# Optimization experiments

Measured on AMD Instinct MI355X. Metric: run time of the kernel, lower is better.

Reference implementation:

```python
import jax, jax.numpy as jnp
import numpy as np

IN_CH, OUT_CH, K, STRIDE = 128, 256, 3, 1

def setup_inputs() -> dict:
    key = jax.random.key(0)
    kx, kw = jax.random.split(key)
    x = jax.random.normal(kx, (32, IN_CH, 56, 56), dtype=jnp.float32)
    # xavier_uniform: bound = sqrt(6 / (fan_in + fan_out)), fans include receptive field
    fan_in = IN_CH * K * K
    fan_out = OUT_CH * K * K
    bound = float(np.sqrt(6.0 / (fan_in + fan_out)))
    weight = jax.random.uniform(kw, (OUT_CH, IN_CH, K, K), dtype=jnp.float32,
                                minval=-bound, maxval=bound)
    bias = jnp.zeros((OUT_CH,), dtype=jnp.float32)
    return {"x": x, "weight": weight, "bias": bias}

def reference(x, weight, bias):
    # VALID (no-padding) conv, stride STRIDE, NCHW layout, OIHW kernel
    out = jax.lax.conv_general_dilated(
        x, weight,
        window_strides=(STRIDE, STRIDE),
        padding="VALID",
        dimension_numbers=("NCHW", "OIHW", "NCHW"))
    return out + bias[None, :, None, None]
```

## Files before the change

### kernel.cpp

```cpp
#include <hip/hip_runtime.h>
#include <hip/hip_bf16.h>
#include <stdint.h>

#define NB    32
#define CIN   128
#define HIN   56
#define HW    (HIN*HIN)
#define OCH   256
#define OHW   54
#define SPB   (OHW*OHW)
#define KSZ   (CIN*9)
#define BM    256
#define BN    128
#define BK    32
#define NKS   (KSZ/BK)
#define TOTC  (NB*SPB)
#define NT    729
#define GRAN  1536

typedef __attribute__((ext_vector_type(8))) short bf16x8;
typedef __attribute__((ext_vector_type(4))) float f32x4;

typedef __attribute__((address_space(1))) const uint32_t g_u32;
typedef __attribute__((address_space(3))) uint32_t l_u32;
static __device__ __forceinline__ void gl_lds16(const void* g, void* l) {
    __builtin_amdgcn_global_load_lds((g_u32*)g, (l_u32*)l, 16, 0, 0);
}

__global__ void xpose_cast(const float* __restrict__ x, __hip_bfloat16* __restrict__ xt) {
    __shared__ float tile[32][33];
    const int hw0 = blockIdx.x * 32;
    const int c0  = blockIdx.y * 32;
    const int n   = blockIdx.z;
    const int tx = threadIdx.x, ty = threadIdx.y;
    const float* xp = x + ((size_t)n*CIN + c0)*HW + hw0;
    #pragma unroll
    for (int i = ty; i < 32; i += 8)
        tile[i][tx] = xp[(size_t)i*HW + tx];
    __syncthreads();
    const int t = ty*32 + tx;
    const int hwl = t >> 3, q = t & 7;
    ushort4 v;
    v.x = __bfloat16_as_ushort(__float2bfloat16(tile[q*4+0][hwl]));
    v.y = __bfloat16_as_ushort(__float2bfloat16(tile[q*4+1][hwl]));
    v.z = __bfloat16_as_ushort(__float2bfloat16(tile[q*4+2][hwl]));
    v.w = __bfloat16_as_ushort(__float2bfloat16(tile[q*4+3][hwl]));
    __hip_bfloat16* op = xt + ((size_t)n*HW + hw0 + hwl)*CIN + c0 + q*4;
    *(ushort4*)op = v;
}

__global__ void wcast(const float* __restrict__ w, __hip_bfloat16* __restrict__ wt) {
    int tid = blockIdx.x*256 + threadIdx.x;
    if (tid >= OCH*KSZ) return;
    int oc = tid / KSZ, r = tid % KSZ;
    int pos = r >> 7, ic = r & 127;
    wt[tid] = __float2bfloat16(w[((size_t)(oc*CIN + ic))*9 + pos]);
}

__global__ __launch_bounds__(256, 2)
void conv_mfma(const __hip_bfloat16* __restrict__ xt,
               const __hip_bfloat16* __restrict__ wt,
               const float* __restrict__ bias,
               float* __restrict__ out) {
    __shared__ uint4 smem[3*GRAN];

    const int t = threadIdx.x;
    const int orig = blockIdx.x;
    const int xcd = orig & 7;
    const int tile = (xcd < 1 ? xcd*92 : 92 + (xcd-1)*91) + (orig >> 3);

    const int lane = t & 63, wid = t >> 6;
    const int wm = wid >> 1, wn = wid & 1;
    const int lr = lane & 15, lq = lane >> 4;

    const __hip_bfloat16* asrc[4];
    #pragma unroll
    for (int i = 0; i < 4; ++i) {
        int q = i*256 + t;
        int row = q >> 2, j = q & 3;
        int ls = j ^ ((row >> 1) & 3);
        asrc[i] = wt + (size_t)row*KSZ + ls*8;
    }
    const __hip_bfloat16* bsrc[2];
    #pragma unroll
    for (int i = 0; i < 2; ++i) {
        int q = i*256 + t;
        int col = q >> 2, j = q & 3;
        int ls = j ^ ((col >> 1) & 3);
        int colg = tile*BN + col;
        int n = colg / SPB, rem = colg - n*SPB;
        int oh = rem / OHW, ow = rem - oh*OHW;
        bsrc[i] = xt + ((size_t)(n*HIN + oh)*HIN + ow)*CIN + ls*8;
    }

    auto issueT = [&](uint4* dst, int ks) {
        const int aoff = ks*BK;
        const int pos = ks >> 2;
        const int kh = pos / 3, kw = pos - kh*3;
        const int boff = (kh*HIN + kw)*CIN + (ks & 3)*32;
        #pragma unroll
        for (int i = 0; i < 4; ++i) gl_lds16(asrc[i] + aoff, dst + i*256 + t);
        #pragma unroll
        for (int i = 0; i < 2; ++i) gl_lds16(bsrc[i] + boff, dst + 1024 + i*256 + t);
    };

    int ao[8], bo[4];
    #pragma unroll
    for (int mi = 0; mi < 8; ++mi) {
        int ra = wm*128 + mi*16 + lr;
        ao[mi] = ra*4 + (lq ^ ((ra >> 1) & 3));
    }
    #pragma unroll
    for (int ni = 0; ni < 4; ++ni) {
        int cb = wn*64 + ni*16 + lr;
        bo[ni] = 1024 + cb*4 + (lq ^ ((cb >> 1) & 3));
    }

    f32x4 acc[8][4];
    #pragma unroll
    for (int i = 0; i < 8; ++i)
        #pragma unroll
        for (int j = 0; j < 4; ++j)
            acc[i][j] = (f32x4){0.f, 0.f, 0.f, 0.f};

    #define MFMA_BF16 __builtin_amdgcn_mfma_f32_16x16x32_bf16
    #define RD_AABB(AA, BB, P) \
        _Pragma("unroll") for (int mi = 0; mi < 4; ++mi) AA[mi] = *(bf16x8*)&(P)[ao[mi]]; \
        _Pragma("unroll") for (int ni = 0; ni < 4; ++ni) BB[ni] = *(bf16x8*)&(P)[bo[ni]];
    #define RD_AB(AB, P) \
        _Pragma("unroll") for (int mi = 0; mi < 4; ++mi) AB[mi] = *(bf16x8*)&(P)[ao[4 + mi]];
    #define MFMA16LO(AA, BB) \
        _Pragma("unroll") for (int mi = 0; mi < 4; ++mi) \
            _Pragma("unroll") for (int ni = 0; ni < 4; ++ni) \
                acc[mi][ni] = MFMA_BF16(AA[mi], BB[ni], acc[mi][ni], 0, 0, 0);
    #define MFMA16HI(AB, BB) \
        _Pragma("unroll") for (int mi = 0; mi < 4; ++mi) \
            _Pragma("unroll") for (int ni = 0; ni < 4; ++ni) \
                acc[4+mi][ni] = MFMA_BF16(AB[mi], BB[ni], acc[4+mi][ni], 0, 0, 0);
    #define SCHEDB __builtin_amdgcn_sched_barrier(0)

    uint4 *bcur = smem, *bnext = smem + GRAN, *bthird = smem + 2*GRAN;
    bf16x8 aaE[4], abE[4], bbE[4];
    bf16x8 aaO[4], abO[4], bbO[4];

    issueT(bcur, 0); issueT(bnext, 1);
    asm volatile("s_waitcnt vmcnt(6)" ::: "memory");
    __builtin_amdgcn_s_barrier();
    SCHEDB;
    RD_AABB(aaE, bbE, bcur)
    RD_AB(abE, bcur)

    for (int ks = 0; ks < NKS; ks += 2) {
        asm volatile("s_waitcnt vmcnt(0)" ::: "memory");
        __builtin_amdgcn_s_barrier();
        SCHEDB;
        if (ks + 2 < NKS) issueT(bthird, ks + 2);
        RD_AABB(aaO, bbO, bnext)
        asm volatile("s_waitcnt lgkmcnt(8)" ::: "memory");
        SCHEDB;
        MFMA16LO(aaE, bbE)
        RD_AB(abO, bnext)
        MFMA16HI(abE, bbE)
        { uint4* tmp = bcur; bcur = bnext; bnext = bthird; bthird = tmp; }

        asm volatile("s_waitcnt vmcnt(0)" ::: "memory");
        __builtin_amdgcn_s_barrier();
        SCHEDB;
        if (ks + 3 < NKS) issueT(bthird, ks + 3);
        if (ks + 2 < NKS) {
            RD_AABB(aaE, bbE, bnext)
            asm volatile("s_waitcnt lgkmcnt(8)" ::: "memory");
        } else {
            asm volatile("s_waitcnt lgkmcnt(0)" ::: "memory");
        }
        SCHEDB;
        MFMA16LO(aaO, bbO)
        if (ks + 2 < NKS) { RD_AB(abE, bnext) }
        MFMA16HI(abO, bbO)
        { uint4* tmp = bcur; bcur = bnext; bnext = bthird; bthird = tmp; }
    }

    __syncthreads();

    float (*eps)[132] = (float (*)[132])smem;
    const int cl4 = (t & 31) * 4;
    const int rsub = t >> 5;
    const int colg = tile*BN + cl4;
    const int nn = colg / SPB;
    const int sp = colg - nn*SPB;
    #pragma unroll
    for (int h = 0; h < 4; ++h) {
        if (wm == (h >> 1)) {
            const int mib = (h & 1) * 4;
            #pragma unroll
            for (int ii = 0; ii < 4; ++ii) {
                int rl = ii*16 + lq*4;
                #pragma unroll
                for (int ni = 0; ni < 4; ++ni) {
                    int cl = wn*64 + ni*16 + lr;
                    #pragma unroll
                    for (int r = 0; r < 4; ++r)
                        eps[rl + r][cl] = acc[mib + ii][ni][r];
                }
            }
        }
        __syncthreads();
        {
            #pragma unroll
            for (int pass = 0; pass < 8; ++pass) {
                int rl = pass*8 + rsub;
                int rg = h*64 + rl;
                f32x4 v = *(f32x4*)&eps[rl][cl4];
                v = v + bias[rg];
                *(f32x4*)&out[((size_t)nn*OCH + rg)*SPB + sp] = v;
            }
        }
        __syncthreads();
    }
}

__global__ void conv_naive(const float* __restrict__ x, const float* __restrict__ w,
                           const float* __restrict__ bias, float* __restrict__ out) {
    size_t tid = (size_t)blockIdx.x*256 + threadIdx.x;
    const size_t total = (size_t)NB*OCH*SPB;
    if (tid >= total) return;
    int col = (int)(tid % SPB);
    int oc  = (int)((tid / SPB) % OCH);
    int n   = (int)(tid / ((size_t)SPB*OCH));
    int oh = col / OHW, ow = col % OHW;
    float s = bias[oc];
    for (int ic = 0; ic < CIN; ++ic)
        #pragma unroll
        for (int kh = 0; kh < 3; ++kh)
            #pragma unroll
            for (int kw = 0; kw < 3; ++kw)
                s += x[((size_t)(n*CIN+ic)*HIN + oh+kh)*HIN + ow+kw]
                   * w[((size_t)(oc*CIN+ic)*3 + kh)*3 + kw];
    out[tid] = s;
}

extern "C" void kernel_launch(void* const* d_in, const int* in_sizes, int n_in,
                              void* d_out, int out_size, void* d_ws, size_t ws_size,
                              hipStream_t stream) {
    const float* x    = (const float*)d_in[0];
    const float* w    = (const float*)d_in[1];
    const float* bias = (const float*)d_in[2];
    float* out = (float*)d_out;

    const size_t xt_bytes = (size_t)NB*HW*CIN*sizeof(__hip_bfloat16);
    const size_t wt_bytes = (size_t)OCH*KSZ*sizeof(__hip_bfloat16);

    if (ws_size >= xt_bytes + wt_bytes) {
        __hip_bfloat16* xt  = (__hip_bfloat16*)d_ws;
        __hip_bfloat16* wtp = (__hip_bfloat16*)((char*)d_ws + xt_bytes);
        hipLaunchKernelGGL(xpose_cast, dim3(HW/32, CIN/32, NB), dim3(32, 8), 0, stream, x, xt);
        hipLaunchKernelGGL(wcast, dim3((OCH*KSZ + 255)/256), dim3(256), 0, stream, w, wtp);
        hipLaunchKernelGGL(conv_mfma, dim3(NT), dim3(256), 0, stream, xt, wtp, bias, out);
    } else {
        size_t total = (size_t)NB*OCH*SPB;
        hipLaunchKernelGGL(conv_naive, dim3((unsigned)((total + 255)/256)), dim3(256), 0, stream,
                           x, w, bias, out);
    }
}
```

Baseline: 96.31 us.

## Reorder pipelined main loop to overlap LDS reads with MFMA and raise MFMA priority

Restructures the triple-buffered K loop. Each half-step now issues the global prefetch, runs the first MFMA group, reads the next stage's full fragment set from LDS, runs the second MFMA group, and ends with a combined vmcnt/lgkmcnt drain plus barrier. Barriers previously came before the LDS reads; now they come after compute, so LDS reads overlap with MFMAs. It also wraps the MFMA blocks in s_setprio(1)/s_setprio(0) to favour matrix issue across waves, at the cost of full drains at each barrier and more live fragment registers.

```diff
diff --git a/kernel.cpp b/kernel.cpp
--- a/kernel.cpp
+++ b/kernel.cpp
@@ -124,60 +124,52 @@
             acc[i][j] = (f32x4){0.f, 0.f, 0.f, 0.f};
 
     #define MFMA_BF16 __builtin_amdgcn_mfma_f32_16x16x32_bf16
-    #define RD_AABB(AA, BB, P) \
+    #define RDSET(AA, AB, BB, P) \
         _Pragma("unroll") for (int mi = 0; mi < 4; ++mi) AA[mi] = *(bf16x8*)&(P)[ao[mi]]; \
-        _Pragma("unroll") for (int ni = 0; ni < 4; ++ni) BB[ni] = *(bf16x8*)&(P)[bo[ni]];
-    #define RD_AB(AB, P) \
+        _Pragma("unroll") for (int ni = 0; ni < 4; ++ni) BB[ni] = *(bf16x8*)&(P)[bo[ni]]; \
         _Pragma("unroll") for (int mi = 0; mi < 4; ++mi) AB[mi] = *(bf16x8*)&(P)[ao[4 + mi]];
-    #define MFMA16LO(AA, BB) \
+    #define MFMA16(AARR, BARR, MIB) \
+        __builtin_amdgcn_s_setprio(1); \
         _Pragma("unroll") for (int mi = 0; mi < 4; ++mi) \
             _Pragma("unroll") for (int ni = 0; ni < 4; ++ni) \
-                acc[mi][ni] = MFMA_BF16(AA[mi], BB[ni], acc[mi][ni], 0, 0, 0);
-    #define MFMA16HI(AB, BB) \
-        _Pragma("unroll") for (int mi = 0; mi < 4; ++mi) \
-            _Pragma("unroll") for (int ni = 0; ni < 4; ++ni) \
-                acc[4+mi][ni] = MFMA_BF16(AB[mi], BB[ni], acc[4+mi][ni], 0, 0, 0);
+                acc[(MIB)+mi][ni] = MFMA_BF16(AARR[mi], BARR[ni], acc[(MIB)+mi][ni], 0, 0, 0); \
+        __builtin_amdgcn_s_setprio(0);
     #define SCHEDB __builtin_amdgcn_sched_barrier(0)
-
-    uint4 *bcur = smem, *bnext = smem + GRAN, *bthird = smem + 2*GRAN;
+    #define DRAIN_BARRIER() \
+        asm volatile("s_waitcnt vmcnt(0) lgkmcnt(0)" ::: "memory"); \
+        __builtin_amdgcn_s_barrier(); \
+        SCHEDB;
+
+    uint4 *pR = smem, *pN = smem + GRAN, *pS = smem + 2*GRAN;
     bf16x8 aaE[4], abE[4], bbE[4];
     bf16x8 aaO[4], abO[4], bbO[4];
 
-    issueT(bcur, 0); issueT(bnext, 1);
-    asm volatile("s_waitcnt vmcnt(6)" ::: "memory");
-    __builtin_amdgcn_s_barrier();
+    issueT(pR, 0); issueT(pN, 1);
+    DRAIN_BARRIER()
+    RDSET(aaE, abE, bbE, pR)
+    asm volatile("s_waitcnt lgkmcnt(0)" ::: "memory");
     SCHEDB;
-    RD_AABB(aaE, bbE, bcur)
-    RD_AB(abE, bcur)
 
     for (int ks = 0; ks < NKS; ks += 2) {
-        asm volatile("s_waitcnt vmcnt(0)" ::: "memory");
-        __builtin_amdgcn_s_barrier();
+        if (ks + 2 < NKS) issueT(pS, ks + 2);
+        MFMA16(aaE, bbE, 0)
+        RDSET(aaO, abO, bbO, pN)
         SCHEDB;
-        if (ks + 2 < NKS) issueT(bthird, ks + 2);
-        RD_AABB(aaO, bbO, bnext)
-        asm volatile("s_waitcnt lgkmcnt(8)" ::: "memory");
+        MFMA16(abE, bbE, 4)
+        DRAIN_BARRIER()
+        { uint4* t0 = pR; pR = pN; pN = pS; pS = t0; }
+
+        if (ks + 3 < NKS) issueT(pS, ks + 3);
+        MFMA16(aaO, bbO, 0)
+        if (ks + 2 < NKS) { RDSET(aaE, abE, bbE, pN) }
         SCHEDB;
-        MFMA16LO(aaE, bbE)
-        RD_AB(abO, bnext)
-        MFMA16HI(abE, bbE)
-        { uint4* tmp = bcur; bcur = bnext; bnext = bthird; bthird = tmp; }
-
-        asm volatile("s_waitcnt vmcnt(0)" ::: "memory");
-        __builtin_amdgcn_s_barrier();
-        SCHEDB;
-        if (ks + 3 < NKS) issueT(bthird, ks + 3);
+        MFMA16(abO, bbO, 4)
         if (ks + 2 < NKS) {
-            RD_AABB(aaE, bbE, bnext)
-            asm volatile("s_waitcnt lgkmcnt(8)" ::: "memory");
+            DRAIN_BARRIER()
         } else {
             asm volatile("s_waitcnt lgkmcnt(0)" ::: "memory");
         }
-        SCHEDB;
-        MFMA16LO(aaO, bbO)
-        if (ks + 2 < NKS) { RD_AB(abE, bnext) }
-        MFMA16HI(abO, bbO)
-        { uint4* tmp = bcur; bcur = bnext; bnext = bthird; bthird = tmp; }
+        { uint4* t0 = pR; pR = pN; pN = pS; pS = t0; }
     }
 
     __syncthreads();
```

Measured after the change: 97.92 us. About the same (+1.7%).
